# Performance work log

Hardware: AMD Instinct MI355X
Metric: run time of the kernel (lower is better)

The kernel has to match this reference:

```python
import jax, jax.numpy as jnp
import numpy as np

K = 5          # number of spline bins
B = 5.0        # tail bound
HIDDEN = 8
MIN_W = 1e-3; MIN_H = 1e-3; MIN_D = 1e-3  # RQS defaults (Durkan et al.)


def setup_inputs() -> dict:
    n, d = 32768, 64
    L = d - 1
    P = 3 * K - 1
    ks = jax.random.split(jax.random.key(0), 8)
    x = jax.random.normal(ks[0], (n, d), jnp.float32) * 2.0
    init_param = jax.random.uniform(ks[1], (P,), jnp.float32, -0.5, 0.5)
    # ragged first layers: layer l (predicts dim l+1) sees x[:, :l+1]; zero-pad to width L
    mask = (jnp.arange(L)[None, :] <= jnp.arange(L)[:, None]).astype(jnp.float32)
    W1 = jax.random.normal(ks[2], (L, L, HIDDEN), jnp.float32) * 0.2 * mask[:, :, None]
    b1 = jax.random.normal(ks[3], (L, HIDDEN), jnp.float32) * 0.1
    W2 = jax.random.normal(ks[4], (L, HIDDEN, HIDDEN), jnp.float32) * 0.2
    b2 = jax.random.normal(ks[5], (L, HIDDEN), jnp.float32) * 0.1
    W3 = jax.random.normal(ks[6], (L, HIDDEN, P), jnp.float32) * 0.2
    b3 = jax.random.normal(ks[7], (L, P), jnp.float32) * 0.1
    return {"x": x, "init_param": init_param, "W1": W1, "b1": b1,
            "W2": W2, "b2": b2, "W3": W3, "b3": b3}


def _rqs(xf, Wu, Hu, Du):
    # xf: (M,), Wu/Hu: (M,K), Du: (M,K-1) -- vectorized unconstrained RQS, forward
    inside = (xf >= -B) & (xf <= B)
    const = float(np.log(np.exp(1.0 - MIN_D) - 1.0))
    Dpad = jnp.pad(Du, ((0, 0), (1, 1)), constant_values=const)

    widths = MIN_W + (1.0 - MIN_W * K) * jax.nn.softmax(Wu, axis=-1)
    cumw = jnp.pad(jnp.cumsum(widths, -1), ((0, 0), (1, 0)))
    cumw = 2.0 * B * cumw - B
    cumw = cumw.at[:, 0].set(-B).at[:, -1].set(B)
    widths = cumw[:, 1:] - cumw[:, :-1]

    heights = MIN_H + (1.0 - MIN_H * K) * jax.nn.softmax(Hu, axis=-1)
    cumh = jnp.pad(jnp.cumsum(heights, -1), ((0, 0), (1, 0)))
    cumh = 2.0 * B * cumh - B
    cumh = cumh.at[:, 0].set(-B).at[:, -1].set(B)
    heights = cumh[:, 1:] - cumh[:, :-1]

    derivs = MIN_D + jax.nn.softplus(Dpad)  # (M, K+1)

    xc = jnp.clip(xf, -B, B)
    idx = jnp.clip(jnp.sum(xc[:, None] >= cumw, axis=-1) - 1, 0, K - 1)
    take = lambda a: jnp.take_along_axis(a, idx[:, None], axis=-1)[:, 0]

    icw, ibw = take(cumw), take(widths)
    ich, ih = take(cumh), take(heights)
    idl = take(heights / widths)
    idv = take(derivs)
    idvp1 = take(derivs[:, 1:])

    theta = (xc - icw) / ibw
    tmt = theta * (1.0 - theta)
    num = ih * (idl * theta * theta + idv * tmt)
    den = idl + (idv + idvp1 - 2.0 * idl) * tmt
    out = ich + num / den
    dnum = idl * idl * (idvp1 * theta * theta + 2.0 * idl * tmt + idv * (1.0 - theta) ** 2)
    ld = jnp.log(dnum) - 2.0 * jnp.log(den)
    return jnp.where(inside, out, xf), jnp.where(inside, ld, 0.0)


def reference(x, init_param, W1, b1, W2, b2, W3, b3):
    n, d = x.shape
    L = d - 1
    P = 3 * K - 1
    # mask re-applied so padded W1 entries are exactly inert (ragged Linear(i, hidden))
    mask = (jnp.arange(L)[None, :] <= jnp.arange(L)[:, None]).astype(x.dtype)
    h = jnp.tanh(jnp.einsum('nj,ljh->lnh', x[:, :L], W1 * mask[:, :, None]) + b1[:, None, :])
    h = jnp.tanh(jnp.einsum('lnh,lhg->lng', h, W2) + b2[:, None, :])
    out = jnp.einsum('lng,lgp->lnp', h, W3) + b3[:, None, :]      # (L, n, P)
    p0 = jnp.broadcast_to(init_param, (1, n, P))                  # dim 0 uses init_param
    params = jnp.concatenate([p0, out], axis=0).reshape(d * n, P)  # dim-major, matches Ws layout
    Wu, Hu, Du = params[:, :K], params[:, K:2 * K], params[:, 2 * K:]
    xf = x.T.reshape(-1)  # x.transpose(0,1).flatten()
    zs, lds = _rqs(xf, Wu, Hu, Du)
    # NOTE: faithfully replicates the original's reshape of the dim-major flat
    # vector directly to (n, d) (as in the torch source).
    return zs.reshape(n, d), lds.reshape(n, d).sum(axis=1)
```

## Files before the change

### kernel.cpp

```cpp
#include <hip/hip_runtime.h>
#include <hip/hip_bf16.h>
#include <math.h>

#define KK 5
#define Bc 5.0f
#define NN 32768
#define DD 64
#define LL 63
#define PP 14
#define MIN_Wc 0.001f
#define MIN_Hc 0.001f
#define MIN_Dc 0.001f
#define LOG2E 1.44269504088896340736f
#define TWOLOG2E 2.88539008177792681472f
#define LN2 0.69314718055994530942f

typedef float f4 __attribute__((ext_vector_type(4)));
typedef float f32x4 __attribute__((ext_vector_type(4)));
typedef float f2 __attribute__((ext_vector_type(2)));
typedef short short8 __attribute__((ext_vector_type(8)));

__device__ __forceinline__ float rcp_fast(float v)   { return __builtin_amdgcn_rcpf(v); }
__device__ __forceinline__ float exp2_fast(float v)  { return __builtin_amdgcn_exp2f(v); }
__device__ __forceinline__ float log2_fast(float v)  { return __builtin_amdgcn_logf(v); }
__device__ __forceinline__ float tanh_pre(float t2) {
    float e = exp2_fast(t2);
    return 1.0f - 2.0f * rcp_fast(e + 1.0f);
}
__device__ __forceinline__ float softplus2(float v2) {
    return (v2 > 21.7f) ? LN2 * v2 : LN2 * log2_fast(1.0f + exp2_fast(v2));
}
__device__ __forceinline__ ushort to_bf16t(float v) {
    return (ushort)(__float_as_uint(v) >> 16);
}
__device__ __forceinline__ unsigned pack_bf16t2(float v0, float v1) {
    return (__float_as_uint(v0) >> 16) | (__float_as_uint(v1) & 0xFFFF0000u);
}
__device__ __forceinline__ float bflo(unsigned u) { return __uint_as_float(u << 16); }
__device__ __forceinline__ float bfhi(unsigned u) { return __uint_as_float(u & 0xFFFF0000u); }
__device__ __forceinline__ f2 splat2(float v) { f2 r; r.x = v; r.y = v; return r; }
__device__ __forceinline__ f4 splat4(float v) { f4 r; r.x = v; r.y = v; r.z = v; r.w = v; return r; }

__device__ __forceinline__ short8 pack_a(f4 v0, f4 v1) {
    short8 a;
    a[0] = (short)to_bf16t(v0.x); a[1] = (short)to_bf16t(v0.y);
    a[2] = (short)to_bf16t(v0.z); a[3] = (short)to_bf16t(v0.w);
    a[4] = (short)to_bf16t(v1.x); a[5] = (short)to_bf16t(v1.y);
    a[6] = (short)to_bf16t(v1.z); a[7] = (short)to_bf16t(v1.w);
    return a;
}

#define WSL 216
#define H1S 72
#define BS  72


__device__ __forceinline__ void do_dim2(
    int dd, const float* wp, float xf0, float xf1, uint4 hv0, uint4 hv1,
    int s0, int lane, int bx,
    const float* __restrict__ ip, float* __restrict__ out)
{
    float h0_0 = bflo(hv0.x), h1_0 = bflo(hv1.x);
    float h0_1 = bfhi(hv0.x), h1_1 = bfhi(hv1.x);
    float h0_2 = bflo(hv0.y), h1_2 = bflo(hv1.y);
    float h0_3 = bfhi(hv0.y), h1_3 = bfhi(hv1.y);
    float h0_4 = bflo(hv0.z), h1_4 = bflo(hv1.z);
    float h0_5 = bfhi(hv0.z), h1_5 = bfhi(hv1.z);
    float h0_6 = bflo(hv0.w), h1_6 = bflo(hv1.w);
    float h0_7 = bfhi(hv0.w), h1_7 = bfhi(hv1.w);

    f4 a0 = *(const f4*)(wp + 64), b0 = *(const f4*)(wp + 68);
    f4 a1 = a0, b1 = b0;
#define L2STEP(HI, X0, X1) { \
    f4 wa = *(const f4*)(wp + (HI) * 8); \
    f4 wb = *(const f4*)(wp + (HI) * 8 + 4); \
    f4 v0 = splat4(X0), v1 = splat4(X1); \
    a0 += v0 * wa; a1 += v1 * wa; \
    b0 += v0 * wb; b1 += v1 * wb; }
    L2STEP(0, h0_0, h1_0)
    L2STEP(1, h0_1, h1_1)
    L2STEP(2, h0_2, h1_2)
    L2STEP(3, h0_3, h1_3)
    L2STEP(4, h0_4, h1_4)
    L2STEP(5, h0_5, h1_5)
    L2STEP(6, h0_6, h1_6)
    L2STEP(7, h0_7, h1_7)
#undef L2STEP
    float g0_0 = tanh_pre(a0.x), g1_0 = tanh_pre(a1.x);
    float g0_1 = tanh_pre(a0.y), g1_1 = tanh_pre(a1.y);
    float g0_2 = tanh_pre(a0.z), g1_2 = tanh_pre(a1.z);
    float g0_3 = tanh_pre(a0.w), g1_3 = tanh_pre(a1.w);
    float g0_4 = tanh_pre(b0.x), g1_4 = tanh_pre(b1.x);
    float g0_5 = tanh_pre(b0.y), g1_5 = tanh_pre(b1.y);
    float g0_6 = tanh_pre(b0.z), g1_6 = tanh_pre(b1.z);
    float g0_7 = tanh_pre(b0.w), g1_7 = tanh_pre(b1.w);

    f4 pa0 = *(const f4*)(wp + 200), pb0 = *(const f4*)(wp + 204);
    f4 pc0 = *(const f4*)(wp + 208), pd0 = *(const f4*)(wp + 212);
    f4 pa1 = pa0, pb1 = pb0, pc1 = pc0, pd1 = pd0;
#define L3STEP(GI, X0, X1) { \
    const float* wr = wp + 72 + (GI) * 16; \
    f4 w0 = *(const f4*)(wr); \
    f4 w1 = *(const f4*)(wr + 4); \
    f4 w2 = *(const f4*)(wr + 8); \
    f4 w3 = *(const f4*)(wr + 12); \
    f4 v0 = splat4(X0), v1 = splat4(X1); \
    pa0 += v0 * w0; pa1 += v1 * w0; \
    pb0 += v0 * w1; pb1 += v1 * w1; \
    pc0 += v0 * w2; pc1 += v1 * w2; \
    pd0 += v0 * w3; pd1 += v1 * w3; }
    L3STEP(0, g0_0, g1_0)
    L3STEP(1, g0_1, g1_1)
    L3STEP(2, g0_2, g1_2)
    L3STEP(3, g0_3, g1_3)
    L3STEP(4, g0_4, g1_4)
    L3STEP(5, g0_5, g1_5)
    L3STEP(6, g0_6, g1_6)
    L3STEP(7, g0_7, g1_7)
#undef L3STEP

    float p0_0 = pa0.x, p0_1 = pa0.y, p0_2 = pa0.z, p0_3 = pa0.w;
    float p0_4 = pb0.x, p0_5 = pb0.y, p0_6 = pb0.z, p0_7 = pb0.w;
    float p0_8 = pc0.x, p0_9 = pc0.y, p0_10 = pc0.z, p0_11 = pc0.w;
    float p0_12 = pd0.x, p0_13 = pd0.y;
    float p1_0 = pa1.x, p1_1 = pa1.y, p1_2 = pa1.z, p1_3 = pa1.w;
    float p1_4 = pb1.x, p1_5 = pb1.y, p1_6 = pb1.z, p1_7 = pb1.w;
    float p1_8 = pc1.x, p1_9 = pc1.y, p1_10 = pc1.z, p1_11 = pc1.w;
    float p1_12 = pd1.x, p1_13 = pd1.y;

    if (dd == 0) {
        p0_0 = LOG2E * ip[0];  p0_1 = LOG2E * ip[1];  p0_2 = LOG2E * ip[2];
        p0_3 = LOG2E * ip[3];  p0_4 = LOG2E * ip[4];  p0_5 = LOG2E * ip[5];
        p0_6 = LOG2E * ip[6];  p0_7 = LOG2E * ip[7];  p0_8 = LOG2E * ip[8];
        p0_9 = LOG2E * ip[9];  p0_10 = LOG2E * ip[10]; p0_11 = LOG2E * ip[11];
        p0_12 = LOG2E * ip[12]; p0_13 = LOG2E * ip[13];
        p1_0 = p0_0;  p1_1 = p0_1;  p1_2 = p0_2;  p1_3 = p0_3;
        p1_4 = p0_4;  p1_5 = p0_5;  p1_6 = p0_6;  p1_7 = p0_7;
        p1_8 = p0_8;  p1_9 = p0_9;  p1_10 = p0_10; p1_11 = p0_11;
        p1_12 = p0_12; p1_13 = p0_13;
    }

    f4 e0, e1, e2, e3, e4;
    e0.x = exp2_fast(p0_0); e0.y = exp2_fast(p0_5); e0.z = exp2_fast(p1_0); e0.w = exp2_fast(p1_5);
    e1.x = exp2_fast(p0_1); e1.y = exp2_fast(p0_6); e1.z = exp2_fast(p1_1); e1.w = exp2_fast(p1_6);
    e2.x = exp2_fast(p0_2); e2.y = exp2_fast(p0_7); e2.z = exp2_fast(p1_2); e2.w = exp2_fast(p1_7);
    e3.x = exp2_fast(p0_3); e3.y = exp2_fast(p0_8); e3.z = exp2_fast(p1_3); e3.w = exp2_fast(p1_8);
    e4.x = exp2_fast(p0_4); e4.y = exp2_fast(p0_9); e4.z = exp2_fast(p1_4); e4.w = exp2_fast(p1_9);
    f4 es = (e0 + e1) + (e2 + e3) + e4;
    f4 nrm;
    nrm.x = 0.995f * rcp_fast(es.x); nrm.y = 0.995f * rcp_fast(es.y);
    nrm.z = 0.995f * rcp_fast(es.z); nrm.w = 0.995f * rcp_fast(es.w);

    const f4 minv = {MIN_Wc, MIN_Hc, MIN_Wc, MIN_Hc};
    f4 acc4 = splat4(0.f);
    acc4 += minv + nrm * e0;  f4 cb1 = splat4(2.f * Bc) * acc4 - splat4(Bc);
    acc4 += minv + nrm * e1;  f4 cb2 = splat4(2.f * Bc) * acc4 - splat4(Bc);
    acc4 += minv + nrm * e2;  f4 cb3 = splat4(2.f * Bc) * acc4 - splat4(Bc);
    acc4 += minv + nrm * e3;  f4 cb4 = splat4(2.f * Bc) * acc4 - splat4(Bc);

    const float xc0 = fminf(fmaxf(xf0, -Bc), Bc);
    const float xc1 = fminf(fmaxf(xf1, -Bc), Bc);

    float icw0 = -Bc, ich0 = -Bc, hw0 = cb1.x, hh0 = cb1.y;
    float icw1 = -Bc, ich1 = -Bc, hw1 = cb1.z, hh1 = cb1.w;
    float rv0 = p0_10, rvp0 = p0_10, rv1 = p1_10, rvp1 = p1_10;
    bool vone0 = true, vpone0 = false, vone1 = true, vpone1 = false;
    {
        bool c0 = xc0 >= cb1.x;               bool c1 = xc1 >= cb1.z;
        icw0 = c0 ? cb1.x : icw0;             icw1 = c1 ? cb1.z : icw1;
        ich0 = c0 ? cb1.y : ich0;             ich1 = c1 ? cb1.w : ich1;
        hw0  = c0 ? cb2.x : hw0;              hw1  = c1 ? cb2.z : hw1;
        hh0  = c0 ? cb2.y : hh0;              hh1  = c1 ? cb2.w : hh1;
        vone0 = c0 ? false : vone0;           vone1 = c1 ? false : vone1;
        rv0  = c0 ? p0_10 : rv0;              rv1  = c1 ? p1_10 : rv1;
        rvp0 = c0 ? p0_11 : rvp0;             rvp1 = c1 ? p1_11 : rvp1;
    }
    {
        bool c0 = xc0 >= cb2.x;               bool c1 = xc1 >= cb2.z;
        icw0 = c0 ? cb2.x : icw0;             icw1 = c1 ? cb2.z : icw1;
        ich0 = c0 ? cb2.y : ich0;             ich1 = c1 ? cb2.w : ich1;
        hw0  = c0 ? cb3.x : hw0;              hw1  = c1 ? cb3.z : hw1;
        hh0  = c0 ? cb3.y : hh0;              hh1  = c1 ? cb3.w : hh1;
        rv0  = c0 ? p0_11 : rv0;              rv1  = c1 ? p1_11 : rv1;
        rvp0 = c0 ? p0_12 : rvp0;             rvp1 = c1 ? p1_12 : rvp1;
    }
    {
        bool c0 = xc0 >= cb3.x;               bool c1 = xc1 >= cb3.z;
        icw0 = c0 ? cb3.x : icw0;             icw1 = c1 ? cb3.z : icw1;
        ich0 = c0 ? cb3.y : ich0;             ich1 = c1 ? cb3.w : ich1;
        hw0  = c0 ? cb4.x : hw0;              hw1  = c1 ? cb4.z : hw1;
        hh0  = c0 ? cb4.y : hh0;              hh1  = c1 ? cb4.w : hh1;
        rv0  = c0 ? p0_12 : rv0;              rv1  = c1 ? p1_12 : rv1;
        rvp0 = c0 ? p0_13 : rvp0;             rvp1 = c1 ? p1_13 : rvp1;
    }
    {
        bool c0 = xc0 >= cb4.x;               bool c1 = xc1 >= cb4.z;
        icw0 = c0 ? cb4.x : icw0;             icw1 = c1 ? cb4.z : icw1;
        ich0 = c0 ? cb4.y : ich0;             ich1 = c1 ? cb4.w : ich1;
        hw0  = c0 ? Bc : hw0;                 hw1  = c1 ? Bc : hw1;
        hh0  = c0 ? Bc : hh0;                 hh1  = c1 ? Bc : hh1;
        rv0  = c0 ? p0_13 : rv0;              rv1  = c1 ? p1_13 : rv1;
        vpone0 = c0;                          vpone1 = c1;
    }
    const float ibw0 = hw0 - icw0, ih0 = hh0 - ich0;
    const float ibw1 = hw1 - icw1, ih1 = hh1 - ich1;
    const float idv0   = vone0  ? 1.0f : MIN_Dc + softplus2(rv0);
    const float idv1   = vone1  ? 1.0f : MIN_Dc + softplus2(rv1);
    const float idvp0  = vpone0 ? 1.0f : MIN_Dc + softplus2(rvp0);
    const float idvp1_ = vpone1 ? 1.0f : MIN_Dc + softplus2(rvp1);

    const float ibr0 = rcp_fast(ibw0);        const float ibr1 = rcp_fast(ibw1);
    const float idl0 = ih0 * ibr0;            const float idl1 = ih1 * ibr1;
    const float th0 = (xc0 - icw0) * ibr0;    const float th1 = (xc1 - icw1) * ibr1;
    const float om0 = 1.0f - th0;             const float om1 = 1.0f - th1;
    const float tm0 = th0 * om0;              const float tm1 = th1 * om1;
    const float num0 = ih0 * (idl0 * th0 * th0 + idv0 * tm0);
    const float num1 = ih1 * (idl1 * th1 * th1 + idv1 * tm1);
    const float den0 = idl0 + (idv0 + idvp0 - 2.0f * idl0) * tm0;
    const float den1 = idl1 + (idv1 + idvp1_ - 2.0f * idl1) * tm1;
    const float dr0 = rcp_fast(den0);         const float dr1 = rcp_fast(den1);
    const float out0 = ich0 + num0 * dr0;     const float out1v = ich1 + num1 * dr1;
    const float dn0 = idl0 * idl0 * (idvp0 * th0 * th0 + 2.0f * idl0 * tm0 + idv0 * om0 * om0);
    const float dn1 = idl1 * idl1 * (idvp1_ * th1 * th1 + 2.0f * idl1 * tm1 + idv1 * om1 * om1);
    const float ld0 = LN2 * log2_fast(dn0 * dr0 * dr0);
    const float ld1 = LN2 * log2_fast(dn1 * dr1 * dr1);

    const bool in0 = (xf0 >= -Bc) && (xf0 <= Bc);
    const bool in1 = (xf1 >= -Bc) && (xf1 <= Bc);
    const float z0 = in0 ? out0 : xf0;        const float z1 = in1 ? out1v : xf1;
    float lv0 = in0 ? ld0 : 0.0f;             float lv1 = in1 ? ld1 : 0.0f;

    out[dd * NN + s0 + lane] = z0;
    out[dd * NN + s0 + 64 + lane] = z1;

    #pragma unroll
    for (int off = 32; off > 0; off >>= 1) {
        lv0 += __shfl_down(lv0, off);
        lv1 += __shfl_down(lv1, off);
    }
    if (lane == 0) {
        out[NN * DD + dd * (NN / 64) + 2 * bx]     = lv0;
        out[NN * DD + dd * (NN / 64) + 2 * bx + 1] = lv1;
    }
}

__device__ __forceinline__ void stage_wl(
    int tid, int l0, float* wl,
    const float* __restrict__ W2, const float* __restrict__ b2,
    const float* __restrict__ W3, const float* __restrict__ b3)
{
    if (tid < 128) {
        int s = tid >> 4, o = (tid & 15) * 4;
        if (l0 + s < LL)
            *(f4*)&wl[s * WSL + o] = splat4(TWOLOG2E) * (*(const f4*)&W2[(l0 + s) * 64 + o]);
    }
    if (tid < 64) {
        int s = tid >> 3, o = tid & 7;
        if (l0 + s < LL) wl[s * WSL + 64 + o] = TWOLOG2E * b2[(l0 + s) * 8 + o];
    }
    #pragma unroll
    for (int q0 = 0; q0 < 448; q0 += 256) {
        int q = q0 + tid;
        if (q < 448) {
            int s = q / 56, r = q % 56, g = r / 7, o = r % 7;
            if (l0 + s < LL)
                *(f2*)&wl[s * WSL + 72 + g * 16 + o * 2] =
                    splat2(LOG2E) * (*(const f2*)&W3[(l0 + s) * 112 + g * 14 + o * 2]);
        }
    }
    if (tid < 64) {
        int s = tid >> 3, g = tid & 7;
        *(f2*)&wl[s * WSL + 72 + g * 16 + 14] = splat2(0.f);
    }
    if (tid < 112) {
        int s = tid / 14, o = tid % 14;
        wl[s * WSL + 200 + o] = LOG2E * b3[(l0 + s < LL ? l0 + s : 0) * PP + o];
    }
    if (tid < 16) {
        int s = tid >> 1, o = 214 + (tid & 1);
        wl[s * WSL + o] = 0.f;
    }
}

__global__ __launch_bounds__(256) void pack_b1(
    const float* __restrict__ W1, unsigned* __restrict__ Bp)
{
    int id = blockIdx.x * 256 + threadIdx.x;
    int n = id >> 5;
    int kw = id & 31;
    int l = n >> 3, h = n & 7;
    const float* src = W1 + (size_t)l * 63 * 8 + h;
    int k0 = 2 * kw, k1 = k0 + 1;
    float v0 = (n < 504 && k0 < 63) ? src[(size_t)k0 * 8] : 0.f;
    float v1 = (n < 504 && k1 < 63) ? src[(size_t)k1 * 8] : 0.f;
    Bp[id] = pack_bf16t2(v0, v1);
}

__global__ __launch_bounds__(256, 4) void fused_kernel(
    const float* __restrict__ x, const float* __restrict__ init_param,
    const ushort* __restrict__ Bp, const float* __restrict__ b1,
    const float* __restrict__ W2, const float* __restrict__ b2,
    const float* __restrict__ W3, const float* __restrict__ b3,
    float* __restrict__ out)
{
    __shared__ ushort h1c[128 * H1S];
    __shared__ float  wl[8 * WSL];
    const int tid = threadIdx.x;
    const int s0 = blockIdx.x * 128;
    const int y  = blockIdx.y;
    const int bx = blockIdx.x;
    const int lane = tid & 63;
    const int wave = __builtin_amdgcn_readfirstlane(tid >> 6);
    const int ln = lane & 15, qg = lane >> 4;
    const int l0 = y * 8;

    const int dA = y * 8 + 1 + 2 * wave;
    const int dB = (y == 7 && wave == 3) ? 0 : dA + 1;
    const float* xr0 = x + (size_t)(s0 + lane) * 64;
    const float* xr1 = xr0 + 64 * 64;
    float xA0 = xr0[dA], xA1 = xr1[dA];
    float xB0 = xr0[dB], xB1 = xr1[dB];

    short8 a0_0, a1_0, a0_1, a1_1;
    {
        const float* p0 = x + (size_t)(s0 + wave * 16 + ln) * 64 + qg * 8;
        const float* p1 = p0 + 64 * 64;
        a0_0 = pack_a(*(const f4*)p0, *(const f4*)(p0 + 4));
        a0_1 = pack_a(*(const f4*)p1, *(const f4*)(p1 + 4));
        if (y >= 4) {
            a1_0 = pack_a(*(const f4*)(p0 + 32), *(const f4*)(p0 + 36));
            a1_1 = pack_a(*(const f4*)(p1 + 32), *(const f4*)(p1 + 36));
        } else { a1_0 = a0_0; a1_1 = a0_1; }
    }

    stage_wl(tid, l0, wl, W2, b2, W3, b3);

    #pragma unroll 2
    for (int nt = 0; nt < 4; ++nt) {
        int ncol = y * 64 + nt * 16 + ln;
        const ushort* brow = Bp + (size_t)ncol * 64 + qg * 8;
        short8 bf0 = *(const short8*)brow;
        f32x4 acc0 = {0.f, 0.f, 0.f, 0.f};
        f32x4 acc1 = {0.f, 0.f, 0.f, 0.f};
        acc0 = __builtin_amdgcn_mfma_f32_16x16x32_bf16(a0_0, bf0, acc0, 0, 0, 0);
        acc1 = __builtin_amdgcn_mfma_f32_16x16x32_bf16(a0_1, bf0, acc1, 0, 0, 0);
        if (y >= 4) {
            short8 bf1 = *(const short8*)(brow + 32);
            acc0 = __builtin_amdgcn_mfma_f32_16x16x32_bf16(a1_0, bf1, acc0, 0, 0, 0);
            acc1 = __builtin_amdgcn_mfma_f32_16x16x32_bf16(a1_1, bf1, acc1, 0, 0, 0);
        }
        float bias2 = (ncol < 504) ? TWOLOG2E * b1[ncol] : 0.f;
        #pragma unroll
        for (int r = 0; r < 4; ++r) {
            int row = wave * 16 + qg * 4 + r;
            float v0 = tanh_pre(fmaf(TWOLOG2E, acc0[r], bias2));
            float v1 = tanh_pre(fmaf(TWOLOG2E, acc1[r], bias2));
            h1c[row * H1S + nt * 16 + ln] = to_bf16t(v0);
            h1c[(row + 64) * H1S + nt * 16 + ln] = to_bf16t(v1);
        }
    }
    __syncthreads();

    const int slA = 2 * wave, slB = 2 * wave + 1;
    uint4 hA0 = *(const uint4*)&h1c[lane * H1S + slA * 8];
    uint4 hA1 = *(const uint4*)&h1c[(lane + 64) * H1S + slA * 8];
    uint4 hB0 = *(const uint4*)&h1c[lane * H1S + slB * 8];
    uint4 hB1 = *(const uint4*)&h1c[(lane + 64) * H1S + slB * 8];

    do_dim2(dA, wl + slA * WSL, xA0, xA1, hA0, hA1, s0, lane, bx, init_param, out);
    do_dim2(dB, wl + slB * WSL, xB0, xB1, hB0, hB1, s0, lane, bx, init_param, out);
}

__global__ __launch_bounds__(256, 4) void fused_kernel_lds(
    const float* __restrict__ x, const float* __restrict__ init_param,
    const float* __restrict__ W1, const float* __restrict__ b1,
    const float* __restrict__ W2, const float* __restrict__ b2,
    const float* __restrict__ W3, const float* __restrict__ b3,
    float* __restrict__ out)
{
    __shared__ ushort h1c[128 * H1S];
    __shared__ float  wl[8 * WSL];
    __shared__ ushort Blds[64 * BS];
    const int tid = threadIdx.x;
    const int s0 = blockIdx.x * 128;
    const int y  = blockIdx.y;
    const int bx = blockIdx.x;
    const int lane = tid & 63;
    const int wave = __builtin_amdgcn_readfirstlane(tid >> 6);
    const int ln = lane & 15, qg = lane >> 4;
    const int l0 = y * 8;

    const int dA = y * 8 + 1 + 2 * wave;
    const int dB = (y == 7 && wave == 3) ? 0 : dA + 1;
    const float* xr0 = x + (size_t)(s0 + lane) * 64;
    const float* xr1 = xr0 + 64 * 64;
    float xA0 = xr0[dA], xA1 = xr1[dA];
    float xB0 = xr0[dB], xB1 = xr1[dB];

    short8 a0_0, a1_0, a0_1, a1_1;
    {
        const float* p0 = x + (size_t)(s0 + wave * 16 + ln) * 64 + qg * 8;
        const float* p1 = p0 + 64 * 64;
        a0_0 = pack_a(*(const f4*)p0, *(const f4*)(p0 + 4));
        a0_1 = pack_a(*(const f4*)p1, *(const f4*)(p1 + 4));
        if (y >= 4) {
            a1_0 = pack_a(*(const f4*)(p0 + 32), *(const f4*)(p0 + 36));
            a1_1 = pack_a(*(const f4*)(p1 + 32), *(const f4*)(p1 + 36));
        } else { a1_0 = a0_0; a1_1 = a0_1; }
    }

    {
        const int n_local = tid >> 2;
        const int n = y * 64 + n_local;
        const int l = n >> 3, h = n & 7;
        const float* src = W1 + (size_t)l * 63 * 8 + h;
        unsigned* drow = (unsigned*)&Blds[n_local * BS];
        if (y < 4) {
            const int kc0 = (tid & 3) * 8;
            #pragma unroll
            for (int j = 0; j < 4; ++j) {
                int k = kc0 + 2 * j;
                float v0 = src[(size_t)k * 8];
                float v1 = src[(size_t)(k + 1) * 8];
                drow[(kc0 >> 1) + j] = pack_bf16t2(v0, v1);
            }
        } else {
            const int kc0 = (tid & 3) * 16;
            #pragma unroll
            for (int j = 0; j < 8; ++j) {
                int k = kc0 + 2 * j;
                float v0 = (n < 504 && k < 63)     ? src[(size_t)k * 8]       : 0.f;
                float v1 = (n < 504 && k + 1 < 63) ? src[(size_t)(k + 1) * 8] : 0.f;
                drow[(kc0 >> 1) + j] = pack_bf16t2(v0, v1);
            }
        }
    }

    stage_wl(tid, l0, wl, W2, b2, W3, b3);
    __syncthreads();

    #pragma unroll
    for (int nt = 0; nt < 4; ++nt) {
        int ncol = y * 64 + nt * 16 + ln;
        const ushort* brow = &Blds[(nt * 16 + ln) * BS + qg * 8];
        short8 bf0 = *(const short8*)brow;
        f32x4 acc0 = {0.f, 0.f, 0.f, 0.f};
        f32x4 acc1 = {0.f, 0.f, 0.f, 0.f};
        acc0 = __builtin_amdgcn_mfma_f32_16x16x32_bf16(a0_0, bf0, acc0, 0, 0, 0);
        acc1 = __builtin_amdgcn_mfma_f32_16x16x32_bf16(a0_1, bf0, acc1, 0, 0, 0);
        if (y >= 4) {
            short8 bf1 = *(const short8*)(brow + 32);
            acc0 = __builtin_amdgcn_mfma_f32_16x16x32_bf16(a1_0, bf1, acc0, 0, 0, 0);
            acc1 = __builtin_amdgcn_mfma_f32_16x16x32_bf16(a1_1, bf1, acc1, 0, 0, 0);
        }
        float bias2 = (ncol < 504) ? TWOLOG2E * b1[ncol] : 0.f;
        #pragma unroll
        for (int r = 0; r < 4; ++r) {
            int row = wave * 16 + qg * 4 + r;
            float v0 = tanh_pre(fmaf(TWOLOG2E, acc0[r], bias2));
            float v1 = tanh_pre(fmaf(TWOLOG2E, acc1[r], bias2));
            h1c[row * H1S + nt * 16 + ln] = to_bf16t(v0);
            h1c[(row + 64) * H1S + nt * 16 + ln] = to_bf16t(v1);
        }
    }
    __syncthreads();

    const int slA = 2 * wave, slB = 2 * wave + 1;
    uint4 hA0 = *(const uint4*)&h1c[lane * H1S + slA * 8];
    uint4 hA1 = *(const uint4*)&h1c[(lane + 64) * H1S + slA * 8];
    uint4 hB0 = *(const uint4*)&h1c[lane * H1S + slB * 8];
    uint4 hB1 = *(const uint4*)&h1c[(lane + 64) * H1S + slB * 8];

    do_dim2(dA, wl + slA * WSL, xA0, xA1, hA0, hA1, s0, lane, bx, init_param, out);
    do_dim2(dB, wl + slB * WSL, xB0, xB1, hB0, hB1, s0, lane, bx, init_param, out);
}

extern "C" void kernel_launch(void* const* d_in, const int* in_sizes, int n_in,
                              void* d_out, int out_size, void* d_ws, size_t ws_size,
                              hipStream_t stream) {
    const float* x          = (const float*)d_in[0];
    const float* init_param = (const float*)d_in[1];
    const float* W1         = (const float*)d_in[2];
    const float* b1         = (const float*)d_in[3];
    const float* W2         = (const float*)d_in[4];
    const float* b2         = (const float*)d_in[5];
    const float* W3         = (const float*)d_in[6];
    const float* b3         = (const float*)d_in[7];
    float* out = (float*)d_out;

    if (d_ws != nullptr && ws_size >= 512 * 64 * sizeof(ushort)) {
        unsigned* Bp = (unsigned*)d_ws;
        pack_b1<<<64, 256, 0, stream>>>(W1, Bp);
        fused_kernel<<<dim3(256, 8), 256, 0, stream>>>(x, init_param,
                                                       (const ushort*)Bp, b1,
                                                       W2, b2, W3, b3, out);
    } else {
        fused_kernel_lds<<<dim3(256, 8), 256, 0, stream>>>(x, init_param, W1, b1,
                                                           W2, b2, W3, b3, out);
    }
}
```

Measured before the change: 105.7 us.

## Double block size so each wave handles one output dimension

```diff
diff --git a/kernel.cpp b/kernel.cpp
--- a/kernel.cpp
+++ b/kernel.cpp
@@ -258,15 +258,11 @@
         int s = tid >> 3, o = tid & 7;
         if (l0 + s < LL) wl[s * WSL + 64 + o] = TWOLOG2E * b2[(l0 + s) * 8 + o];
     }
-    #pragma unroll
-    for (int q0 = 0; q0 < 448; q0 += 256) {
-        int q = q0 + tid;
-        if (q < 448) {
-            int s = q / 56, r = q % 56, g = r / 7, o = r % 7;
-            if (l0 + s < LL)
-                *(f2*)&wl[s * WSL + 72 + g * 16 + o * 2] =
-                    splat2(LOG2E) * (*(const f2*)&W3[(l0 + s) * 112 + g * 14 + o * 2]);
-        }
+    if (tid < 448) {
+        int s = tid / 56, r = tid % 56, g = r / 7, o = r % 7;
+        if (l0 + s < LL)
+            *(f2*)&wl[s * WSL + 72 + g * 16 + o * 2] =
+                splat2(LOG2E) * (*(const f2*)&W3[(l0 + s) * 112 + g * 14 + o * 2]);
     }
     if (tid < 64) {
         int s = tid >> 3, g = tid & 7;
@@ -296,7 +292,7 @@
     Bp[id] = pack_bf16t2(v0, v1);
 }
 
-__global__ __launch_bounds__(256, 4) void fused_kernel(
+__global__ __launch_bounds__(512, 8) void fused_kernel(
     const float* __restrict__ x, const float* __restrict__ init_param,
     const ushort* __restrict__ Bp, const float* __restrict__ b1,
     const float* __restrict__ W2, const float* __restrict__ b2,
@@ -314,23 +310,17 @@
     const int ln = lane & 15, qg = lane >> 4;
     const int l0 = y * 8;
 
-    const int dA = y * 8 + 1 + 2 * wave;
-    const int dB = (y == 7 && wave == 3) ? 0 : dA + 1;
-    const float* xr0 = x + (size_t)(s0 + lane) * 64;
-    const float* xr1 = xr0 + 64 * 64;
-    float xA0 = xr0[dA], xA1 = xr1[dA];
-    float xB0 = xr0[dB], xB1 = xr1[dB];
-
-    short8 a0_0, a1_0, a0_1, a1_1;
-    {
-        const float* p0 = x + (size_t)(s0 + wave * 16 + ln) * 64 + qg * 8;
-        const float* p1 = p0 + 64 * 64;
-        a0_0 = pack_a(*(const f4*)p0, *(const f4*)(p0 + 4));
-        a0_1 = pack_a(*(const f4*)p1, *(const f4*)(p1 + 4));
-        if (y >= 4) {
-            a1_0 = pack_a(*(const f4*)(p0 + 32), *(const f4*)(p0 + 36));
-            a1_1 = pack_a(*(const f4*)(p1 + 32), *(const f4*)(p1 + 36));
-        } else { a1_0 = a0_0; a1_1 = a0_1; }
+    const int dd = (y == 7 && wave == 7) ? 0 : y * 8 + 1 + wave;
+    const float xf0 = x[(size_t)(s0 + lane) * 64 + dd];
+    const float xf1 = x[(size_t)(s0 + 64 + lane) * 64 + dd];
+
+    short8 a0, a1;
+    {
+        const int rbase = (wave & 3) * 16 + ((wave >= 4) ? 64 : 0);
+        const float* p0 = x + (size_t)(s0 + rbase + ln) * 64 + qg * 8;
+        a0 = pack_a(*(const f4*)p0, *(const f4*)(p0 + 4));
+        if (y >= 4) a1 = pack_a(*(const f4*)(p0 + 32), *(const f4*)(p0 + 36));
+        else        a1 = a0;
     }
 
     stage_wl(tid, l0, wl, W2, b2, W3, b3);
@@ -340,35 +330,26 @@
         int ncol = y * 64 + nt * 16 + ln;
         const ushort* brow = Bp + (size_t)ncol * 64 + qg * 8;
         short8 bf0 = *(const short8*)brow;
-        f32x4 acc0 = {0.f, 0.f, 0.f, 0.f};
-        f32x4 acc1 = {0.f, 0.f, 0.f, 0.f};
-        acc0 = __builtin_amdgcn_mfma_f32_16x16x32_bf16(a0_0, bf0, acc0, 0, 0, 0);
-        acc1 = __builtin_amdgcn_mfma_f32_16x16x32_bf16(a0_1, bf0, acc1, 0, 0, 0);
+        f32x4 acc = {0.f, 0.f, 0.f, 0.f};
+        acc = __builtin_amdgcn_mfma_f32_16x16x32_bf16(a0, bf0, acc, 0, 0, 0);
         if (y >= 4) {
             short8 bf1 = *(const short8*)(brow + 32);
-            acc0 = __builtin_amdgcn_mfma_f32_16x16x32_bf16(a1_0, bf1, acc0, 0, 0, 0);
-            acc1 = __builtin_amdgcn_mfma_f32_16x16x32_bf16(a1_1, bf1, acc1, 0, 0, 0);
+            acc = __builtin_amdgcn_mfma_f32_16x16x32_bf16(a1, bf1, acc, 0, 0, 0);
         }
         float bias2 = (ncol < 504) ? TWOLOG2E * b1[ncol] : 0.f;
         #pragma unroll
         for (int r = 0; r < 4; ++r) {
             int row = wave * 16 + qg * 4 + r;
-            float v0 = tanh_pre(fmaf(TWOLOG2E, acc0[r], bias2));
-            float v1 = tanh_pre(fmaf(TWOLOG2E, acc1[r], bias2));
-            h1c[row * H1S + nt * 16 + ln] = to_bf16t(v0);
-            h1c[(row + 64) * H1S + nt * 16 + ln] = to_bf16t(v1);
+            h1c[row * H1S + nt * 16 + ln] =
+                to_bf16t(tanh_pre(fmaf(TWOLOG2E, acc[r], bias2)));
         }
     }
     __syncthreads();
 
-    const int slA = 2 * wave, slB = 2 * wave + 1;
-    uint4 hA0 = *(const uint4*)&h1c[lane * H1S + slA * 8];
-    uint4 hA1 = *(const uint4*)&h1c[(lane + 64) * H1S + slA * 8];
-    uint4 hB0 = *(const uint4*)&h1c[lane * H1S + slB * 8];
-    uint4 hB1 = *(const uint4*)&h1c[(lane + 64) * H1S + slB * 8];
-
-    do_dim2(dA, wl + slA * WSL, xA0, xA1, hA0, hA1, s0, lane, bx, init_param, out);
-    do_dim2(dB, wl + slB * WSL, xB0, xB1, hB0, hB1, s0, lane, bx, init_param, out);
+    uint4 hv0 = *(const uint4*)&h1c[lane * H1S + wave * 8];
+    uint4 hv1 = *(const uint4*)&h1c[(lane + 64) * H1S + wave * 8];
+
+    do_dim2(dd, wl + wave * WSL, xf0, xf1, hv0, hv1, s0, lane, bx, init_param, out);
 }
 
 __global__ __launch_bounds__(256, 4) void fused_kernel_lds(
@@ -491,7 +472,7 @@
     if (d_ws != nullptr && ws_size >= 512 * 64 * sizeof(ushort)) {
         unsigned* Bp = (unsigned*)d_ws;
         pack_b1<<<64, 256, 0, stream>>>(W1, Bp);
-        fused_kernel<<<dim3(256, 8), 256, 0, stream>>>(x, init_param,
+        fused_kernel<<<dim3(256, 8), 512, 0, stream>>>(x, init_param,
                                                        (const ushort*)Bp, b1,
                                                        W2, b2, W3, b3, out);
     } else {
```

New measurement: 115.8 us. 1.1x slower.
